# Kernel optimization log

Hardware: AMD Instinct MI355X
Metric: run time of the kernel (lower is better)

## Reference

```python
import jax, jax.numpy as jnp
import numpy as np

B, T, H = 4096, 2048, 64  # batch, max seq len, hidden size
IN = 1                    # decoder input hardcoded to width 1 in source
BOT = 3                   # latent bottleneck (linear_enc: H->3, linear_dec: 3->H)


def setup_inputs() -> dict:
    key = jax.random.key(0)
    ks = jax.random.split(key, 16)
    s = 1.0 / np.sqrt(H)
    u = lambda k, shape: jax.random.uniform(k, shape, jnp.float32, -s, s)
    padded = jax.random.normal(ks[0], (B, T, IN), jnp.float32)
    seq_lengths = jax.random.randint(ks[1], (B,), 1, T + 1).at[0].set(T)  # max == T (static unroll)
    return {
        "padded": padded,
        "seq_lengths": seq_lengths,
        # encoder LSTM (gate order i,f,g,o like torch); biases b_ih+b_hh fused
        "enc_Wih": u(ks[2], (4 * H, IN)),
        "enc_Whh": u(ks[3], (4 * H, H)),
        "enc_b":   u(ks[4], (4 * H,)),
        # encoder bottleneck linear H->3
        "enc_linW": u(ks[5], (BOT, H)),
        "enc_linb": u(ks[6], (BOT,)),
        # decoder expand linear 3->H
        "dec_linW": u(ks[7], (H, BOT)),
        "dec_linb": u(ks[8], (H,)),
        # decoder LSTM
        "dec_Wih": u(ks[9], (4 * H, IN)),
        "dec_Whh": u(ks[10], (4 * H, H)),
        "dec_b":   u(ks[11], (4 * H,)),
        # output linear H->1
        "outW": u(ks[12], (IN, H)),
        "outb": u(ks[13], (IN,)),
    }


def _lstm_cell(x, h, c, Wih, Whh, b):
    g = x @ Wih.T + h @ Whh.T + b
    i, f, gg, o = jnp.split(g, 4, axis=-1)
    c = jax.nn.sigmoid(f) * c + jax.nn.sigmoid(i) * jnp.tanh(gg)
    h = jax.nn.sigmoid(o) * jnp.tanh(c)
    return h, c


def reference(padded, seq_lengths, enc_Wih, enc_Whh, enc_b, enc_linW, enc_linb,
              dec_linW, dec_linb, dec_Wih, dec_Whh, dec_b, outW, outb):
    Bn, Tn, _ = padded.shape
    Hn = enc_Whh.shape[1]
    xs = jnp.transpose(padded, (1, 0, 2))                       # (T, B, 1)
    mask = jnp.arange(Tn)[:, None] < seq_lengths[None, :]        # (T, B)

    # ---- encoder: packed semantics == freeze (h,c) past each seq's length ----
    h0 = jnp.zeros((Bn, Hn), padded.dtype)
    def enc_step(carry, xm):
        h, c = carry
        x, m = xm
        nh, nc = _lstm_cell(x, h, c, enc_Wih, enc_Whh, enc_b)
        m = m[:, None]
        return (jnp.where(m, nh, h), jnp.where(m, nc, c)), None
    (h, c), _ = jax.lax.scan(enc_step, (h0, h0), (xs, mask))

    hz = jax.nn.sigmoid(h @ enc_linW.T + enc_linb)               # (B, 3) latent

    hd = hz @ dec_linW.T + dec_linb                              # (B, H)
    x0 = jnp.zeros((Bn, 1), padded.dtype)
    def dec_step(carry, _):
        x, hh, cc = carry
        nh, nc = _lstm_cell(x, hh, cc, dec_Wih, dec_Whh, dec_b)
        y = nh @ outW.T + outb
        return (y, nh, nc), y
    _, ys = jax.lax.scan(dec_step, (x0, hd, c), None, length=Tn)  # (T, B, 1)
    output = jnp.transpose(ys, (1, 0, 2))                         # (B, T, 1)

    # ---- masked MSE ----
    maskf = mask.T[:, :, None].astype(padded.dtype)               # (B, T, 1)
    loss = (((padded - output) ** 2) * maskf).sum() / maskf.sum()
    return loss, padded, output, hz[None]
```

## Files before the change

### kernel.cpp

```cpp
#include <hip/hip_runtime.h>

#define B 4096
#define T 2048
#define H 64
#define NBATCH 16
#define NB (B / NBATCH)
#define NTHREADS 512

typedef __attribute__((ext_vector_type(8))) short short8;
typedef __attribute__((ext_vector_type(4))) float f32x4;

__device__ __forceinline__ float ex2(float x) { return __builtin_amdgcn_exp2f(x); }
__device__ __forceinline__ unsigned short f2bf(float f) {
    unsigned u = __builtin_bit_cast(unsigned, f);
    u += 0x7fffu + ((u >> 16) & 1u);
    return (unsigned short)(u >> 16);
}
__device__ __forceinline__ unsigned pk_bf16(float a, float b) {
    unsigned r;
    asm("v_cvt_pk_bf16_f32 %0, %1, %2" : "=v"(r) : "v"(a), "v"(b));
    return r;
}
__device__ __forceinline__ void lds_barrier() {
    asm volatile("s_waitcnt lgkmcnt(0)\n\ts_barrier" ::: "memory");
}

__device__ __forceinline__ void cellstep(const f32x4 z, float& cs, float& hs, bool act) {
    const float KE = -1.4426950408889634f;
    const float KT = -2.8853900817779268f;
    float pf = ex2(KE * z[1]);
    float f_ = __builtin_amdgcn_rcpf(1.0f + pf);
    float p0 = ex2(KE * z[0]);
    float v_ = ex2(KT * z[2]);
    float ig = (1.0f - v_) * __builtin_amdgcn_rcpf((1.0f + p0) * (1.0f + v_));
    float cn = __builtin_fmaf(f_, cs, ig);
    float cc = fminf(15.0f, fmaxf(-15.0f, cn));
    float s_ = ex2(KE * z[3]);
    float r_ = ex2(KT * cc);
    float hn = (1.0f - r_) * __builtin_amdgcn_rcpf((1.0f + s_) * (1.0f + r_));
    if (act) { cs = cn; hs = hn; }
}

extern "C" __global__ void __launch_bounds__(NTHREADS, 2)
enc_kernel(const float* __restrict__ padded, const int* __restrict__ seq_len,
           const float* __restrict__ Wih, const float* __restrict__ Whh,
           const float* __restrict__ bias,
           float* __restrict__ h_out, float* __restrict__ c_out)
{
    __shared__ unsigned short hX[2][NBATCH][72];
    __shared__ int slen[NBATCH];

    const int tid = threadIdx.x;
    const int w = tid >> 6, L = tid & 63, lo = L & 15, hi = L >> 4;
    const int b0 = blockIdx.x * NBATCH;
    const int unitA = w * 8 + 2 * hi;
    const int unitB = unitA + 1;

    short8 af[2][2];
    #pragma unroll
    for (int rt = 0; rt < 2; ++rt) {
        const int G = (lo & 3) * 64 + w * 8 + 2 * (lo >> 2) + rt;
        #pragma unroll
        for (int kk = 0; kk < 2; ++kk) {
            const float* src = Whh + (long)G * H + kk * 32 + hi * 8;
            short8 f;
            #pragma unroll
            for (int j = 0; j < 8; ++j) f[j] = (short)f2bf(src[j]);
            af[rt][kk] = f;
        }
    }
    float b_g[2][4], wi_g[2][4];
    #pragma unroll
    for (int rt = 0; rt < 2; ++rt)
        #pragma unroll
        for (int r = 0; r < 4; ++r) {
            const int G2 = r * 64 + w * 8 + 2 * hi + rt;
            b_g[rt][r] = bias[G2];
            wi_g[rt][r] = Wih[G2];
        }

    for (int idx = tid; idx < NBATCH * 64; idx += NTHREADS)
        hX[0][idx >> 6][idx & 63] = 0;
    if (tid < NBATCH) slen[tid] = seq_len[b0 + tid];
    lds_barrier();

    int maxlen = 1;
    #pragma unroll
    for (int i = 0; i < NBATCH; ++i) maxlen = max(maxlen, slen[i]);
    const int len_lo = slen[lo];

    const float* xrow = padded + (long)(b0 + lo) * T;
    f32x4 xc = *(const f32x4*)(xrow);
    f32x4 xn = *(const f32x4*)(xrow + 4);

    float csA = 0.f, hsA = 0.f, csB = 0.f, hsB = 0.f;

#define ESTEP(P, XI)                                                          \
    {                                                                         \
        const float x = xc[XI];                                               \
        short8 hb0 = *(const short8*)&hX[P][lo][hi * 8];                      \
        short8 hb1 = *(const short8*)&hX[P][lo][32 + hi * 8];                 \
        f32x4 z0 = {b_g[0][0] + wi_g[0][0] * x, b_g[0][1] + wi_g[0][1] * x,   \
                    b_g[0][2] + wi_g[0][2] * x, b_g[0][3] + wi_g[0][3] * x};  \
        f32x4 z1 = {b_g[1][0] + wi_g[1][0] * x, b_g[1][1] + wi_g[1][1] * x,   \
                    b_g[1][2] + wi_g[1][2] * x, b_g[1][3] + wi_g[1][3] * x};  \
        z0 = __builtin_amdgcn_mfma_f32_16x16x32_bf16(af[0][0], hb0, z0, 0,0,0); \
        z1 = __builtin_amdgcn_mfma_f32_16x16x32_bf16(af[1][0], hb0, z1, 0,0,0); \
        z0 = __builtin_amdgcn_mfma_f32_16x16x32_bf16(af[0][1], hb1, z0, 0,0,0); \
        z1 = __builtin_amdgcn_mfma_f32_16x16x32_bf16(af[1][1], hb1, z1, 0,0,0); \
        const bool act = (t + XI) < len_lo;                                   \
        cellstep(z0, csA, hsA, act);                                          \
        cellstep(z1, csB, hsB, act);                                          \
        *(unsigned*)&hX[(P) ^ 1][lo][unitA] = pk_bf16(hsA, hsB);              \
        lds_barrier();                                                        \
    }

    for (int t = 0; t < maxlen; t += 4) {
        int nb = t + 8; if (nb > T - 4) nb = T - 4;
        f32x4 xf = *(const f32x4*)(xrow + nb);
        ESTEP(0, 0) ESTEP(1, 1) ESTEP(0, 2) ESTEP(1, 3)
        xc = xn; xn = xf;
    }
#undef ESTEP

    *(float2*)&h_out[(long)(b0 + lo) * H + unitA] = make_float2(hsA, hsB);
    *(float2*)&c_out[(long)(b0 + lo) * H + unitA] = make_float2(csA, csB);
}

extern "C" __global__ void __launch_bounds__(256)
mid_kernel(const float* __restrict__ h_enc,
           const float* __restrict__ eW, const float* __restrict__ eb,
           const float* __restrict__ dW, const float* __restrict__ db,
           const float* __restrict__ outW, const float* __restrict__ outb,
           float* __restrict__ hz_out, float* __restrict__ hd_out,
           float* __restrict__ y0c)
{
    int b = blockIdx.x * blockDim.x + threadIdx.x;
    if (b >= B) return;
    const float* h = h_enc + (long)b * H;
    float hz[3];
    #pragma unroll
    for (int j = 0; j < 3; ++j) {
        float s = eb[j];
        for (int k = 0; k < H; ++k) s += h[k] * eW[j*H + k];
        hz[j] = 1.0f / (1.0f + __builtin_expf(-s));
        hz_out[b*3 + j] = hz[j];
    }
    float y0 = outb[0];
    for (int u = 0; u < H; ++u) {
        float hd = db[u] + hz[0]*dW[u*3] + hz[1]*dW[u*3+1] + hz[2]*dW[u*3+2];
        hd_out[(long)b*H + u] = hd;
        y0 += outW[u] * hd;
    }
    y0c[b] = y0;
}

extern "C" __global__ void __launch_bounds__(NTHREADS, 2)
dec_kernel(const float* __restrict__ hd, const float* __restrict__ c_in,
           const float* __restrict__ Wih, const float* __restrict__ Whh,
           const float* __restrict__ bias, const float* __restrict__ outW,
           const float* __restrict__ outb, const float* __restrict__ y0c,
           float* __restrict__ y_out)
{
    __shared__ unsigned short hX[2][NBATCH][72];

    const int tid = threadIdx.x;
    const int w = tid >> 6, L = tid & 63, lo = L & 15, hi = L >> 4;
    const int b0 = blockIdx.x * NBATCH;
    const int unitA = w * 8 + 2 * hi;
    const int unitB = unitA + 1;

    short8 af[2][2];
    #pragma unroll
    for (int rt = 0; rt < 2; ++rt) {
        const int G = (lo & 3) * 64 + w * 8 + 2 * (lo >> 2) + rt;
        const float wir = Wih[G];
        #pragma unroll
        for (int kk = 0; kk < 2; ++kk) {
            const float* src = Whh + (long)G * H + kk * 32 + hi * 8;
            const float* ow  = outW + kk * 32 + hi * 8;
            short8 f;
            #pragma unroll
            for (int j = 0; j < 8; ++j) f[j] = (short)f2bf(src[j] + wir * ow[j]);
            af[rt][kk] = f;
        }
    }
    const float outb_s = outb[0];
    const float y0 = y0c[b0 + lo];
    float zb[2][4], corr[2][4];
    #pragma unroll
    for (int rt = 0; rt < 2; ++rt)
        #pragma unroll
        for (int r = 0; r < 4; ++r) {
            const int G2 = r * 64 + w * 8 + 2 * hi + rt;
            zb[rt][r] = bias[G2] + Wih[G2] * outb_s;
            corr[rt][r] = Wih[G2] * y0;
        }

    short8 ya[2];
    #pragma unroll
    for (int kk = 0; kk < 2; ++kk) {
        short8 f = (short8)0;
        if (lo == 0)
            #pragma unroll
            for (int j = 0; j < 8; ++j) f[j] = (short)f2bf(outW[kk*32 + hi*8 + j]);
        ya[kk] = f;
    }

    for (int idx = tid; idx < NBATCH * 64; idx += NTHREADS)
        hX[0][idx >> 6][idx & 63] = f2bf(hd[(long)(b0 + (idx >> 6)) * H + (idx & 63)]);
    float2 c2 = *(const float2*)&c_in[(long)(b0 + lo) * H + unitA];
    float csA = c2.x, csB = c2.y, hsA = 0.f, hsB = 0.f;
    lds_barrier();

#define DSTEP(P, CORR, TT)                                                    \
    {                                                                         \
        short8 hb0 = *(const short8*)&hX[P][lo][hi * 8];                      \
        short8 hb1 = *(const short8*)&hX[P][lo][32 + hi * 8];                 \
        f32x4 z0 = {zb[0][0], zb[0][1], zb[0][2], zb[0][3]};                  \
        f32x4 z1 = {zb[1][0], zb[1][1], zb[1][2], zb[1][3]};                  \
        z0 = __builtin_amdgcn_mfma_f32_16x16x32_bf16(af[0][0], hb0, z0, 0,0,0); \
        z1 = __builtin_amdgcn_mfma_f32_16x16x32_bf16(af[1][0], hb0, z1, 0,0,0); \
        z0 = __builtin_amdgcn_mfma_f32_16x16x32_bf16(af[0][1], hb1, z0, 0,0,0); \
        z1 = __builtin_amdgcn_mfma_f32_16x16x32_bf16(af[1][1], hb1, z1, 0,0,0); \
        if (w == ((TT) & 7)) {      \
            f32x4 zy = {outb_s, outb_s, outb_s, outb_s};                      \
            zy = __builtin_amdgcn_mfma_f32_16x16x32_bf16(ya[0], hb0, zy, 0,0,0); \
            zy = __builtin_amdgcn_mfma_f32_16x16x32_bf16(ya[1], hb1, zy, 0,0,0); \
            if ((TT) > 0 && hi == 0)                                          \
                y_out[(long)(b0 + lo) * T + ((TT) - 1)] = zy[0];              \
        }                                                                     \
        if (CORR) {                                                           \
            _Pragma("unroll")                                                 \
            for (int r = 0; r < 4; ++r) { z0[r] -= corr[0][r]; z1[r] -= corr[1][r]; } \
        }                                                                     \
        cellstep(z0, csA, hsA, true);                                         \
        cellstep(z1, csB, hsB, true);                                         \
        *(unsigned*)&hX[(P) ^ 1][lo][unitA] = pk_bf16(hsA, hsB);              \
        lds_barrier();                                                        \
    }

    DSTEP(0, 1, 0) DSTEP(1, 0, 1) DSTEP(0, 0, 2) DSTEP(1, 0, 3)
    for (int t = 4; t < T; t += 4) {
        DSTEP(0, 0, t) DSTEP(1, 0, t + 1) DSTEP(0, 0, t + 2) DSTEP(1, 0, t + 3)
    }
#undef DSTEP

    if (w == 0) {
        short8 hb0 = *(const short8*)&hX[0][lo][hi * 8];
        short8 hb1 = *(const short8*)&hX[0][lo][32 + hi * 8];
        f32x4 zy = {outb_s, outb_s, outb_s, outb_s};
        zy = __builtin_amdgcn_mfma_f32_16x16x32_bf16(ya[0], hb0, zy, 0,0,0);
        zy = __builtin_amdgcn_mfma_f32_16x16x32_bf16(ya[1], hb1, zy, 0,0,0);
        if (hi == 0) y_out[(long)(b0 + lo) * T + (T - 1)] = zy[0];
    }
}

extern "C" __global__ void __launch_bounds__(256)
loss_kernel(const float* __restrict__ padded, const float* __restrict__ y,
            const int* __restrict__ seq_len, float* __restrict__ acc2)
{
    const long n4 = (long)B * T / 4;
    long i0 = (long)(blockIdx.x * blockDim.x + threadIdx.x);
    long stride = (long)gridDim.x * blockDim.x;
    float s = 0.f, cnt = 0.f;
    for (long i = i0; i < n4; i += stride) {
        int b = (int)(i >> 9);
        int t = (int)(i & 511) * 4;
        int len = seq_len[b];
        f32x4 pv = *(const f32x4*)&padded[i * 4];
        f32x4 yv = *(const f32x4*)&y[i * 4];
        #pragma unroll
        for (int e = 0; e < 4; ++e)
            if (t + e < len) { float d = pv[e] - yv[e]; s += d * d; cnt += 1.0f; }
    }
    for (int m = 1; m < 64; m <<= 1) { s += __shfl_xor(s, m); cnt += __shfl_xor(cnt, m); }
    if ((threadIdx.x & 63) == 0) { atomicAdd(&acc2[0], s); atomicAdd(&acc2[1], cnt); }
}

extern "C" __global__ void fin_kernel(const float* __restrict__ acc2, float* __restrict__ out)
{
    out[0] = acc2[0] / acc2[1];
}

extern "C" void kernel_launch(void* const* d_in, const int* in_sizes, int n_in,
                              void* d_out, int out_size, void* d_ws, size_t ws_size,
                              hipStream_t stream)
{
    const float* padded = (const float*)d_in[0];
    const int*   seq    = (const int*)  d_in[1];
    const float* eWih   = (const float*)d_in[2];
    const float* eWhh   = (const float*)d_in[3];
    const float* eb     = (const float*)d_in[4];
    const float* elW    = (const float*)d_in[5];
    const float* elb    = (const float*)d_in[6];
    const float* dlW    = (const float*)d_in[7];
    const float* dlb    = (const float*)d_in[8];
    const float* dWih   = (const float*)d_in[9];
    const float* dWhh   = (const float*)d_in[10];
    const float* db     = (const float*)d_in[11];
    const float* outW   = (const float*)d_in[12];
    const float* outb   = (const float*)d_in[13];
    float* out = (float*)d_out;

    float* ws    = (float*)d_ws;
    float* h_enc = ws;
    float* c_enc = ws + (long)B * H;
    float* hd    = ws + 2L * B * H;
    float* y0c   = ws + 3L * B * H;
    float* acc2  = ws + 3L * B * H + B;

    float* out_pad = out + 1;
    float* out_y   = out + 1 + (long)B * T;
    float* out_hz  = out + 1 + 2L * (long)B * T;

    hipMemcpyAsync(out_pad, padded, (long)B * T * sizeof(float),
                   hipMemcpyDeviceToDevice, stream);
    hipMemsetAsync(acc2, 0, 2 * sizeof(float), stream);

    enc_kernel<<<NB, NTHREADS, 0, stream>>>(padded, seq, eWih, eWhh, eb, h_enc, c_enc);
    mid_kernel<<<B / 256, 256, 0, stream>>>(h_enc, elW, elb, dlW, dlb, outW, outb,
                                            out_hz, hd, y0c);
    dec_kernel<<<NB, NTHREADS, 0, stream>>>(hd, c_enc, dWih, dWhh, db, outW, outb, y0c, out_y);
    loss_kernel<<<1024, 256, 0, stream>>>(padded, out_y, seq, acc2);
    fin_kernel<<<1, 1, 0, stream>>>(acc2, out);
}
```

Before: 1.806 ms.

## Split LSTM blocks into two independent 4-wave groups with LDS counter sync

```diff
diff --git a/kernel.cpp b/kernel.cpp
--- a/kernel.cpp
+++ b/kernel.cpp
@@ -23,6 +23,11 @@
 }
 __device__ __forceinline__ void lds_barrier() {
     asm volatile("s_waitcnt lgkmcnt(0)\n\ts_barrier" ::: "memory");
+}
+__device__ __forceinline__ void gsync(unsigned* c, unsigned tgt, int lane) {
+    if (lane == 0)
+        __hip_atomic_fetch_add(c, 1u, __ATOMIC_RELEASE, __HIP_MEMORY_SCOPE_WORKGROUP);
+    while (__hip_atomic_load(c, __ATOMIC_ACQUIRE, __HIP_MEMORY_SCOPE_WORKGROUP) < tgt) {}
 }
 
 __device__ __forceinline__ void cellstep(const f32x4 z, float& cs, float& hs, bool act) {
@@ -47,72 +52,88 @@
            const float* __restrict__ bias,
            float* __restrict__ h_out, float* __restrict__ c_out)
 {
-    __shared__ unsigned short hX[2][NBATCH][72];
+    __shared__ unsigned short hX[2][2][8][72];
     __shared__ int slen[NBATCH];
+    __shared__ unsigned cnt[2];
 
     const int tid = threadIdx.x;
     const int w = tid >> 6, L = tid & 63, lo = L & 15, hi = L >> 4;
+    const int g = w >> 2, k = w & 3;
     const int b0 = blockIdx.x * NBATCH;
-    const int unitA = w * 8 + 2 * hi;
-    const int unitB = unitA + 1;
-
-    short8 af[2][2];
-    #pragma unroll
-    for (int rt = 0; rt < 2; ++rt) {
-        const int G = (lo & 3) * 64 + w * 8 + 2 * (lo >> 2) + rt;
+    const int cb = lo & 7;
+    const int unitL = 16 * k + 8 * (lo >> 3) + 2 * hi;
+
+    short8 af[4][2];
+    #pragma unroll
+    for (int t4 = 0; t4 < 4; ++t4) {
+        const int G = (lo & 3) * 64 + 16 * k + 8 * (t4 >> 1) + 2 * (lo >> 2) + (t4 & 1);
         #pragma unroll
         for (int kk = 0; kk < 2; ++kk) {
             const float* src = Whh + (long)G * H + kk * 32 + hi * 8;
             short8 f;
             #pragma unroll
             for (int j = 0; j < 8; ++j) f[j] = (short)f2bf(src[j]);
-            af[rt][kk] = f;
+            af[t4][kk] = f;
         }
     }
-    float b_g[2][4], wi_g[2][4];
-    #pragma unroll
-    for (int rt = 0; rt < 2; ++rt)
+    float b_g[4][4], wi_g[4][4];
+    #pragma unroll
+    for (int t4 = 0; t4 < 4; ++t4)
         #pragma unroll
         for (int r = 0; r < 4; ++r) {
-            const int G2 = r * 64 + w * 8 + 2 * hi + rt;
-            b_g[rt][r] = bias[G2];
-            wi_g[rt][r] = Wih[G2];
+            const int G2 = r * 64 + 16 * k + 8 * (t4 >> 1) + 2 * hi + (t4 & 1);
+            b_g[t4][r] = bias[G2];
+            wi_g[t4][r] = Wih[G2];
         }
 
-    for (int idx = tid; idx < NBATCH * 64; idx += NTHREADS)
-        hX[0][idx >> 6][idx & 63] = 0;
+    for (int idx = tid; idx < 2 * 2 * 8 * 72; idx += NTHREADS)
+        ((unsigned short*)hX)[idx] = 0;
     if (tid < NBATCH) slen[tid] = seq_len[b0 + tid];
+    if (tid < 2) cnt[tid] = 0;
     lds_barrier();
+    if (g == 1) __builtin_amdgcn_s_sleep(8);
 
     int maxlen = 1;
     #pragma unroll
-    for (int i = 0; i < NBATCH; ++i) maxlen = max(maxlen, slen[i]);
-    const int len_lo = slen[lo];
-
-    const float* xrow = padded + (long)(b0 + lo) * T;
+    for (int i = 0; i < 8; ++i) maxlen = max(maxlen, slen[g * 8 + i]);
+    const int len_lo = slen[g * 8 + cb];
+
+    const float* xrow = padded + (long)(b0 + g * 8 + cb) * T;
     f32x4 xc = *(const f32x4*)(xrow);
     f32x4 xn = *(const f32x4*)(xrow + 4);
 
     float csA = 0.f, hsA = 0.f, csB = 0.f, hsB = 0.f;
+    unsigned tgt = 0;
 
 #define ESTEP(P, XI)                                                          \
     {                                                                         \
         const float x = xc[XI];                                               \
-        short8 hb0 = *(const short8*)&hX[P][lo][hi * 8];                      \
-        short8 hb1 = *(const short8*)&hX[P][lo][32 + hi * 8];                 \
-        f32x4 z0 = {b_g[0][0] + wi_g[0][0] * x, b_g[0][1] + wi_g[0][1] * x,   \
+        short8 hb0 = *(const short8*)&hX[g][P][cb][hi * 8];                   \
+        short8 hb1 = *(const short8*)&hX[g][P][cb][32 + hi * 8];              \
+        f32x4 q0 = {b_g[0][0] + wi_g[0][0] * x, b_g[0][1] + wi_g[0][1] * x,   \
                     b_g[0][2] + wi_g[0][2] * x, b_g[0][3] + wi_g[0][3] * x};  \
-        f32x4 z1 = {b_g[1][0] + wi_g[1][0] * x, b_g[1][1] + wi_g[1][1] * x,   \
+        f32x4 q1 = {b_g[1][0] + wi_g[1][0] * x, b_g[1][1] + wi_g[1][1] * x,   \
                     b_g[1][2] + wi_g[1][2] * x, b_g[1][3] + wi_g[1][3] * x};  \
-        z0 = __builtin_amdgcn_mfma_f32_16x16x32_bf16(af[0][0], hb0, z0, 0,0,0); \
-        z1 = __builtin_amdgcn_mfma_f32_16x16x32_bf16(af[1][0], hb0, z1, 0,0,0); \
-        z0 = __builtin_amdgcn_mfma_f32_16x16x32_bf16(af[0][1], hb1, z0, 0,0,0); \
-        z1 = __builtin_amdgcn_mfma_f32_16x16x32_bf16(af[1][1], hb1, z1, 0,0,0); \
+        f32x4 q2 = {b_g[2][0] + wi_g[2][0] * x, b_g[2][1] + wi_g[2][1] * x,   \
+                    b_g[2][2] + wi_g[2][2] * x, b_g[2][3] + wi_g[2][3] * x};  \
+        f32x4 q3 = {b_g[3][0] + wi_g[3][0] * x, b_g[3][1] + wi_g[3][1] * x,   \
+                    b_g[3][2] + wi_g[3][2] * x, b_g[3][3] + wi_g[3][3] * x};  \
+        q0 = __builtin_amdgcn_mfma_f32_16x16x32_bf16(af[0][0], hb0, q0, 0,0,0); \
+        q1 = __builtin_amdgcn_mfma_f32_16x16x32_bf16(af[1][0], hb0, q1, 0,0,0); \
+        q2 = __builtin_amdgcn_mfma_f32_16x16x32_bf16(af[2][0], hb0, q2, 0,0,0); \
+        q3 = __builtin_amdgcn_mfma_f32_16x16x32_bf16(af[3][0], hb0, q3, 0,0,0); \
+        q0 = __builtin_amdgcn_mfma_f32_16x16x32_bf16(af[0][1], hb1, q0, 0,0,0); \
+        q1 = __builtin_amdgcn_mfma_f32_16x16x32_bf16(af[1][1], hb1, q1, 0,0,0); \
+        q2 = __builtin_amdgcn_mfma_f32_16x16x32_bf16(af[2][1], hb1, q2, 0,0,0); \
+        q3 = __builtin_amdgcn_mfma_f32_16x16x32_bf16(af[3][1], hb1, q3, 0,0,0); \
+        const bool rep = lo < 8;                                              \
+        f32x4 zA = rep ? q0 : q2;                                             \
+        f32x4 zB = rep ? q1 : q3;                                             \
         const bool act = (t + XI) < len_lo;                                   \
-        cellstep(z0, csA, hsA, act);                                          \
-        cellstep(z1, csB, hsB, act);                                          \
-        *(unsigned*)&hX[(P) ^ 1][lo][unitA] = pk_bf16(hsA, hsB);              \
-        lds_barrier();                                                        \
+        cellstep(zA, csA, hsA, act);                                          \
+        cellstep(zB, csB, hsB, act);                                          \
+        *(unsigned*)&hX[g][(P) ^ 1][cb][unitL] = pk_bf16(hsA, hsB);           \
+        tgt += 4; gsync(&cnt[g], tgt, L);                                     \
     }
 
     for (int t = 0; t < maxlen; t += 4) {
@@ -123,8 +144,8 @@
     }
 #undef ESTEP
 
-    *(float2*)&h_out[(long)(b0 + lo) * H + unitA] = make_float2(hsA, hsB);
-    *(float2*)&c_out[(long)(b0 + lo) * H + unitA] = make_float2(csA, csB);
+    *(float2*)&h_out[(long)(b0 + g * 8 + cb) * H + unitL] = make_float2(hsA, hsB);
+    *(float2*)&c_out[(long)(b0 + g * 8 + cb) * H + unitL] = make_float2(csA, csB);
 }
 
 extern "C" __global__ void __launch_bounds__(256)
@@ -142,7 +163,7 @@
     #pragma unroll
     for (int j = 0; j < 3; ++j) {
         float s = eb[j];
-        for (int k = 0; k < H; ++k) s += h[k] * eW[j*H + k];
+        for (int kq = 0; kq < H; ++kq) s += h[kq] * eW[j*H + kq];
         hz[j] = 1.0f / (1.0f + __builtin_expf(-s));
         hz_out[b*3 + j] = hz[j];
     }
@@ -162,18 +183,20 @@
            const float* __restrict__ outb, const float* __restrict__ y0c,
            float* __restrict__ y_out)
 {
-    __shared__ unsigned short hX[2][NBATCH][72];
+    __shared__ unsigned short hX[2][2][8][72];
+    __shared__ unsigned cnt[2];
 
     const int tid = threadIdx.x;
     const int w = tid >> 6, L = tid & 63, lo = L & 15, hi = L >> 4;
+    const int g = w >> 2, k = w & 3;
     const int b0 = blockIdx.x * NBATCH;
-    const int unitA = w * 8 + 2 * hi;
-    const int unitB = unitA + 1;
-
-    short8 af[2][2];
-    #pragma unroll
-    for (int rt = 0; rt < 2; ++rt) {
-        const int G = (lo & 3) * 64 + w * 8 + 2 * (lo >> 2) + rt;
+    const int cb = lo & 7;
+    const int unitL = 16 * k + 8 * (lo >> 3) + 2 * hi;
+
+    short8 af[4][2];
+    #pragma unroll
+    for (int t4 = 0; t4 < 4; ++t4) {
+        const int G = (lo & 3) * 64 + 16 * k + 8 * (t4 >> 1) + 2 * (lo >> 2) + (t4 & 1);
         const float wir = Wih[G];
         #pragma unroll
         for (int kk = 0; kk < 2; ++kk) {
@@ -182,20 +205,25 @@
             short8 f;
             #pragma unroll
             for (int j = 0; j < 8; ++j) f[j] = (short)f2bf(src[j] + wir * ow[j]);
-            af[rt][kk] = f;
+            af[t4][kk] = f;
         }
     }
     const float outb_s = outb[0];
-    const float y0 = y0c[b0 + lo];
-    float zb[2][4], corr[2][4];
-    #pragma unroll
-    for (int rt = 0; rt < 2; ++rt)
+    const float y0 = y0c[b0 + g * 8 + cb];
+    float zb[4][4];
+    #pragma unroll
+    for (int t4 = 0; t4 < 4; ++t4)
         #pragma unroll
         for (int r = 0; r < 4; ++r) {
-            const int G2 = r * 64 + w * 8 + 2 * hi + rt;
-            zb[rt][r] = bias[G2] + Wih[G2] * outb_s;
-            corr[rt][r] = Wih[G2] * y0;
+            const int G2 = r * 64 + 16 * k + 8 * (t4 >> 1) + 2 * hi + (t4 & 1);
+            zb[t4][r] = bias[G2] + Wih[G2] * outb_s;
         }
+    float corrA[4], corrB[4];
+    #pragma unroll
+    for (int r = 0; r < 4; ++r) {
+        corrA[r] = Wih[r * 64 + unitL] * y0;
+        corrB[r] = Wih[r * 64 + unitL + 1] * y0;
+    }
 
     short8 ya[2];
     #pragma unroll
@@ -207,37 +235,51 @@
         ya[kk] = f;
     }
 
-    for (int idx = tid; idx < NBATCH * 64; idx += NTHREADS)
-        hX[0][idx >> 6][idx & 63] = f2bf(hd[(long)(b0 + (idx >> 6)) * H + (idx & 63)]);
-    float2 c2 = *(const float2*)&c_in[(long)(b0 + lo) * H + unitA];
+    for (int idx = tid; idx < NBATCH * 64; idx += NTHREADS) {
+        int m = idx >> 6, col = idx & 63;
+        hX[m >> 3][0][m & 7][col] = f2bf(hd[(long)(b0 + m) * H + col]);
+    }
+    if (tid < 2) cnt[tid] = 0;
+    float2 c2 = *(const float2*)&c_in[(long)(b0 + g * 8 + cb) * H + unitL];
     float csA = c2.x, csB = c2.y, hsA = 0.f, hsB = 0.f;
     lds_barrier();
+    if (g == 1) __builtin_amdgcn_s_sleep(8);
+    unsigned tgt = 0;
 
 #define DSTEP(P, CORR, TT)                                                    \
     {                                                                         \
-        short8 hb0 = *(const short8*)&hX[P][lo][hi * 8];                      \
-        short8 hb1 = *(const short8*)&hX[P][lo][32 + hi * 8];                 \
-        f32x4 z0 = {zb[0][0], zb[0][1], zb[0][2], zb[0][3]};                  \
-        f32x4 z1 = {zb[1][0], zb[1][1], zb[1][2], zb[1][3]};                  \
-        z0 = __builtin_amdgcn_mfma_f32_16x16x32_bf16(af[0][0], hb0, z0, 0,0,0); \
-        z1 = __builtin_amdgcn_mfma_f32_16x16x32_bf16(af[1][0], hb0, z1, 0,0,0); \
-        z0 = __builtin_amdgcn_mfma_f32_16x16x32_bf16(af[0][1], hb1, z0, 0,0,0); \
-        z1 = __builtin_amdgcn_mfma_f32_16x16x32_bf16(af[1][1], hb1, z1, 0,0,0); \
-        if (w == ((TT) & 7)) {      \
+        short8 hb0 = *(const short8*)&hX[g][P][cb][hi * 8];                   \
+        short8 hb1 = *(const short8*)&hX[g][P][cb][32 + hi * 8];              \
+        f32x4 q0 = {zb[0][0], zb[0][1], zb[0][2], zb[0][3]};                  \
+        f32x4 q1 = {zb[1][0], zb[1][1], zb[1][2], zb[1][3]};                  \
+        f32x4 q2 = {zb[2][0], zb[2][1], zb[2][2], zb[2][3]};                  \
+        f32x4 q3 = {zb[3][0], zb[3][1], zb[3][2], zb[3][3]};                  \
+        q0 = __builtin_amdgcn_mfma_f32_16x16x32_bf16(af[0][0], hb0, q0, 0,0,0); \
+        q1 = __builtin_amdgcn_mfma_f32_16x16x32_bf16(af[1][0], hb0, q1, 0,0,0); \
+        q2 = __builtin_amdgcn_mfma_f32_16x16x32_bf16(af[2][0], hb0, q2, 0,0,0); \
+        q3 = __builtin_amdgcn_mfma_f32_16x16x32_bf16(af[3][0], hb0, q3, 0,0,0); \
+        q0 = __builtin_amdgcn_mfma_f32_16x16x32_bf16(af[0][1], hb1, q0, 0,0,0); \
+        q1 = __builtin_amdgcn_mfma_f32_16x16x32_bf16(af[1][1], hb1, q1, 0,0,0); \
+        q2 = __builtin_amdgcn_mfma_f32_16x16x32_bf16(af[2][1], hb1, q2, 0,0,0); \
+        q3 = __builtin_amdgcn_mfma_f32_16x16x32_bf16(af[3][1], hb1, q3, 0,0,0); \
+        if (k == ((TT) & 3)) {      \
             f32x4 zy = {outb_s, outb_s, outb_s, outb_s};                      \
             zy = __builtin_amdgcn_mfma_f32_16x16x32_bf16(ya[0], hb0, zy, 0,0,0); \
             zy = __builtin_amdgcn_mfma_f32_16x16x32_bf16(ya[1], hb1, zy, 0,0,0); \
-            if ((TT) > 0 && hi == 0)                                          \
-                y_out[(long)(b0 + lo) * T + ((TT) - 1)] = zy[0];              \
+            if ((TT) > 0 && hi == 0 && lo < 8)                                \
+                y_out[(long)(b0 + g * 8 + lo) * T + ((TT) - 1)] = zy[0];      \
         }                                                                     \
+        const bool rep = lo < 8;                                              \
+        f32x4 zA = rep ? q0 : q2;                                             \
+        f32x4 zB = rep ? q1 : q3;                                             \
         if (CORR) {                                                           \
             _Pragma("unroll")                                                 \
-            for (int r = 0; r < 4; ++r) { z0[r] -= corr[0][r]; z1[r] -= corr[1][r]; } \
+            for (int r = 0; r < 4; ++r) { zA[r] -= corrA[r]; zB[r] -= corrB[r]; } \
         }                                                                     \
-        cellstep(z0, csA, hsA, true);                                         \
-        cellstep(z1, csB, hsB, true);                                         \
-        *(unsigned*)&hX[(P) ^ 1][lo][unitA] = pk_bf16(hsA, hsB);              \
-        lds_barrier();                                                        \
+        cellstep(zA, csA, hsA, true);                                         \
+        cellstep(zB, csB, hsB, true);                                         \
+        *(unsigned*)&hX[g][(P) ^ 1][cb][unitL] = pk_bf16(hsA, hsB);           \
+        tgt += 4; gsync(&cnt[g], tgt, L);                                     \
     }
 
     DSTEP(0, 1, 0) DSTEP(1, 0, 1) DSTEP(0, 0, 2) DSTEP(1, 0, 3)
@@ -246,13 +288,13 @@
     }
 #undef DSTEP
 
-    if (w == 0) {
-        short8 hb0 = *(const short8*)&hX[0][lo][hi * 8];
-        short8 hb1 = *(const short8*)&hX[0][lo][32 + hi * 8];
+    if (k == 0) {
+        short8 hb0 = *(const short8*)&hX[g][0][cb][hi * 8];
+        short8 hb1 = *(const short8*)&hX[g][0][cb][32 + hi * 8];
         f32x4 zy = {outb_s, outb_s, outb_s, outb_s};
         zy = __builtin_amdgcn_mfma_f32_16x16x32_bf16(ya[0], hb0, zy, 0,0,0);
         zy = __builtin_amdgcn_mfma_f32_16x16x32_bf16(ya[1], hb1, zy, 0,0,0);
-        if (hi == 0) y_out[(long)(b0 + lo) * T + (T - 1)] = zy[0];
+        if (hi == 0 && lo < 8) y_out[(long)(b0 + g * 8 + lo) * T + (T - 1)] = zy[0];
     }
 }
 
@@ -263,7 +305,7 @@
     const long n4 = (long)B * T / 4;
     long i0 = (long)(blockIdx.x * blockDim.x + threadIdx.x);
     long stride = (long)gridDim.x * blockDim.x;
-    float s = 0.f, cnt = 0.f;
+    float s = 0.f, cntv = 0.f;
     for (long i = i0; i < n4; i += stride) {
         int b = (int)(i >> 9);
         int t = (int)(i & 511) * 4;
@@ -272,10 +314,10 @@
         f32x4 yv = *(const f32x4*)&y[i * 4];
         #pragma unroll
         for (int e = 0; e < 4; ++e)
-            if (t + e < len) { float d = pv[e] - yv[e]; s += d * d; cnt += 1.0f; }
-    }
-    for (int m = 1; m < 64; m <<= 1) { s += __shfl_xor(s, m); cnt += __shfl_xor(cnt, m); }
-    if ((threadIdx.x & 63) == 0) { atomicAdd(&acc2[0], s); atomicAdd(&acc2[1], cnt); }
+            if (t + e < len) { float d = pv[e] - yv[e]; s += d * d; cntv += 1.0f; }
+    }
+    for (int m = 1; m < 64; m <<= 1) { s += __shfl_xor(s, m); cntv += __shfl_xor(cntv, m); }
+    if ((threadIdx.x & 63) == 0) { atomicAdd(&acc2[0], s); atomicAdd(&acc2[1], cntv); }
 }
 
 extern "C" __global__ void fin_kernel(const float* __restrict__ acc2, float* __restrict__ out)
```

Result: slower. 2.155 ms (+19.3%).

## Halve waves per block so each wave computes four gate tiles

Applied to the files above, without the earlier changes.

```diff
diff --git a/kernel.cpp b/kernel.cpp
--- a/kernel.cpp
+++ b/kernel.cpp
@@ -5,7 +5,7 @@
 #define H 64
 #define NBATCH 16
 #define NB (B / NBATCH)
-#define NTHREADS 512
+#define NTHREADS 256
 
 typedef __attribute__((ext_vector_type(8))) short short8;
 typedef __attribute__((ext_vector_type(4))) float f32x4;
@@ -41,7 +41,7 @@
     if (act) { cs = cn; hs = hn; }
 }
 
-extern "C" __global__ void __launch_bounds__(NTHREADS, 2)
+extern "C" __global__ void __launch_bounds__(NTHREADS, 1)
 enc_kernel(const float* __restrict__ padded, const int* __restrict__ seq_len,
            const float* __restrict__ Wih, const float* __restrict__ Whh,
            const float* __restrict__ bias,
@@ -53,30 +53,30 @@
     const int tid = threadIdx.x;
     const int w = tid >> 6, L = tid & 63, lo = L & 15, hi = L >> 4;
     const int b0 = blockIdx.x * NBATCH;
-    const int unitA = w * 8 + 2 * hi;
-    const int unitB = unitA + 1;
-
-    short8 af[2][2];
-    #pragma unroll
-    for (int rt = 0; rt < 2; ++rt) {
-        const int G = (lo & 3) * 64 + w * 8 + 2 * (lo >> 2) + rt;
+    const int uA = 16 * w + 2 * hi;
+    const int uC = uA + 8;
+
+    short8 af[4][2];
+    #pragma unroll
+    for (int q = 0; q < 4; ++q) {
+        const int G = (lo & 3) * 64 + 16 * w + 8 * (q >> 1) + 2 * (lo >> 2) + (q & 1);
         #pragma unroll
         for (int kk = 0; kk < 2; ++kk) {
             const float* src = Whh + (long)G * H + kk * 32 + hi * 8;
             short8 f;
             #pragma unroll
             for (int j = 0; j < 8; ++j) f[j] = (short)f2bf(src[j]);
-            af[rt][kk] = f;
+            af[q][kk] = f;
         }
     }
-    float b_g[2][4], wi_g[2][4];
-    #pragma unroll
-    for (int rt = 0; rt < 2; ++rt)
+    float b_g[4][4], wi_g[4][4];
+    #pragma unroll
+    for (int q = 0; q < 4; ++q)
         #pragma unroll
         for (int r = 0; r < 4; ++r) {
-            const int G2 = r * 64 + w * 8 + 2 * hi + rt;
-            b_g[rt][r] = bias[G2];
-            wi_g[rt][r] = Wih[G2];
+            const int G2 = r * 64 + 16 * w + 8 * (q >> 1) + 2 * hi + (q & 1);
+            b_g[q][r] = bias[G2];
+            wi_g[q][r] = Wih[G2];
         }
 
     for (int idx = tid; idx < NBATCH * 64; idx += NTHREADS)
@@ -93,7 +93,8 @@
     f32x4 xc = *(const f32x4*)(xrow);
     f32x4 xn = *(const f32x4*)(xrow + 4);
 
-    float csA = 0.f, hsA = 0.f, csB = 0.f, hsB = 0.f;
+    float cs0 = 0.f, hs0 = 0.f, cs1 = 0.f, hs1 = 0.f;
+    float cs2 = 0.f, hs2 = 0.f, cs3 = 0.f, hs3 = 0.f;
 
 #define ESTEP(P, XI)                                                          \
     {                                                                         \
@@ -104,14 +105,25 @@
                     b_g[0][2] + wi_g[0][2] * x, b_g[0][3] + wi_g[0][3] * x};  \
         f32x4 z1 = {b_g[1][0] + wi_g[1][0] * x, b_g[1][1] + wi_g[1][1] * x,   \
                     b_g[1][2] + wi_g[1][2] * x, b_g[1][3] + wi_g[1][3] * x};  \
+        f32x4 z2 = {b_g[2][0] + wi_g[2][0] * x, b_g[2][1] + wi_g[2][1] * x,   \
+                    b_g[2][2] + wi_g[2][2] * x, b_g[2][3] + wi_g[2][3] * x};  \
+        f32x4 z3 = {b_g[3][0] + wi_g[3][0] * x, b_g[3][1] + wi_g[3][1] * x,   \
+                    b_g[3][2] + wi_g[3][2] * x, b_g[3][3] + wi_g[3][3] * x};  \
         z0 = __builtin_amdgcn_mfma_f32_16x16x32_bf16(af[0][0], hb0, z0, 0,0,0); \
         z1 = __builtin_amdgcn_mfma_f32_16x16x32_bf16(af[1][0], hb0, z1, 0,0,0); \
+        z2 = __builtin_amdgcn_mfma_f32_16x16x32_bf16(af[2][0], hb0, z2, 0,0,0); \
+        z3 = __builtin_amdgcn_mfma_f32_16x16x32_bf16(af[3][0], hb0, z3, 0,0,0); \
         z0 = __builtin_amdgcn_mfma_f32_16x16x32_bf16(af[0][1], hb1, z0, 0,0,0); \
         z1 = __builtin_amdgcn_mfma_f32_16x16x32_bf16(af[1][1], hb1, z1, 0,0,0); \
+        z2 = __builtin_amdgcn_mfma_f32_16x16x32_bf16(af[2][1], hb1, z2, 0,0,0); \
+        z3 = __builtin_amdgcn_mfma_f32_16x16x32_bf16(af[3][1], hb1, z3, 0,0,0); \
         const bool act = (t + XI) < len_lo;                                   \
-        cellstep(z0, csA, hsA, act);                                          \
-        cellstep(z1, csB, hsB, act);                                          \
-        *(unsigned*)&hX[(P) ^ 1][lo][unitA] = pk_bf16(hsA, hsB);              \
+        cellstep(z0, cs0, hs0, act);                                          \
+        cellstep(z1, cs1, hs1, act);                                          \
+        cellstep(z2, cs2, hs2, act);                                          \
+        cellstep(z3, cs3, hs3, act);                                          \
+        *(unsigned*)&hX[(P) ^ 1][lo][uA] = pk_bf16(hs0, hs1);                 \
+        *(unsigned*)&hX[(P) ^ 1][lo][uC] = pk_bf16(hs2, hs3);                 \
         lds_barrier();                                                        \
     }
 
@@ -123,8 +135,10 @@
     }
 #undef ESTEP
 
-    *(float2*)&h_out[(long)(b0 + lo) * H + unitA] = make_float2(hsA, hsB);
-    *(float2*)&c_out[(long)(b0 + lo) * H + unitA] = make_float2(csA, csB);
+    *(float2*)&h_out[(long)(b0 + lo) * H + uA] = make_float2(hs0, hs1);
+    *(float2*)&h_out[(long)(b0 + lo) * H + uC] = make_float2(hs2, hs3);
+    *(float2*)&c_out[(long)(b0 + lo) * H + uA] = make_float2(cs0, cs1);
+    *(float2*)&c_out[(long)(b0 + lo) * H + uC] = make_float2(cs2, cs3);
 }
 
 extern "C" __global__ void __launch_bounds__(256)
@@ -155,7 +169,7 @@
     y0c[b] = y0;
 }
 
-extern "C" __global__ void __launch_bounds__(NTHREADS, 2)
+extern "C" __global__ void __launch_bounds__(NTHREADS, 1)
 dec_kernel(const float* __restrict__ hd, const float* __restrict__ c_in,
            const float* __restrict__ Wih, const float* __restrict__ Whh,
            const float* __restrict__ bias, const float* __restrict__ outW,
@@ -167,13 +181,13 @@
     const int tid = threadIdx.x;
     const int w = tid >> 6, L = tid & 63, lo = L & 15, hi = L >> 4;
     const int b0 = blockIdx.x * NBATCH;
-    const int unitA = w * 8 + 2 * hi;
-    const int unitB = unitA + 1;
-
-    short8 af[2][2];
-    #pragma unroll
-    for (int rt = 0; rt < 2; ++rt) {
-        const int G = (lo & 3) * 64 + w * 8 + 2 * (lo >> 2) + rt;
+    const int uA = 16 * w + 2 * hi;
+    const int uC = uA + 8;
+
+    short8 af[4][2];
+    #pragma unroll
+    for (int q = 0; q < 4; ++q) {
+        const int G = (lo & 3) * 64 + 16 * w + 8 * (q >> 1) + 2 * (lo >> 2) + (q & 1);
         const float wir = Wih[G];
         #pragma unroll
         for (int kk = 0; kk < 2; ++kk) {
@@ -182,19 +196,19 @@
             short8 f;
             #pragma unroll
             for (int j = 0; j < 8; ++j) f[j] = (short)f2bf(src[j] + wir * ow[j]);
-            af[rt][kk] = f;
+            af[q][kk] = f;
         }
     }
     const float outb_s = outb[0];
     const float y0 = y0c[b0 + lo];
-    float zb[2][4], corr[2][4];
-    #pragma unroll
-    for (int rt = 0; rt < 2; ++rt)
+    float zb[4][4], corr[4][4];
+    #pragma unroll
+    for (int q = 0; q < 4; ++q)
         #pragma unroll
         for (int r = 0; r < 4; ++r) {
-            const int G2 = r * 64 + w * 8 + 2 * hi + rt;
-            zb[rt][r] = bias[G2] + Wih[G2] * outb_s;
-            corr[rt][r] = Wih[G2] * y0;
+            const int G2 = r * 64 + 16 * w + 8 * (q >> 1) + 2 * hi + (q & 1);
+            zb[q][r] = bias[G2] + Wih[G2] * outb_s;
+            corr[q][r] = Wih[G2] * y0;
         }
 
     short8 ya[2];
@@ -209,8 +223,10 @@
 
     for (int idx = tid; idx < NBATCH * 64; idx += NTHREADS)
         hX[0][idx >> 6][idx & 63] = f2bf(hd[(long)(b0 + (idx >> 6)) * H + (idx & 63)]);
-    float2 c2 = *(const float2*)&c_in[(long)(b0 + lo) * H + unitA];
-    float csA = c2.x, csB = c2.y, hsA = 0.f, hsB = 0.f;
+    float2 cA = *(const float2*)&c_in[(long)(b0 + lo) * H + uA];
+    float2 cC = *(const float2*)&c_in[(long)(b0 + lo) * H + uC];
+    float cs0 = cA.x, cs1 = cA.y, cs2 = cC.x, cs3 = cC.y;
+    float hs0 = 0.f, hs1 = 0.f, hs2 = 0.f, hs3 = 0.f;
     lds_barrier();
 
 #define DSTEP(P, CORR, TT)                                                    \
@@ -219,11 +235,17 @@
         short8 hb1 = *(const short8*)&hX[P][lo][32 + hi * 8];                 \
         f32x4 z0 = {zb[0][0], zb[0][1], zb[0][2], zb[0][3]};                  \
         f32x4 z1 = {zb[1][0], zb[1][1], zb[1][2], zb[1][3]};                  \
+        f32x4 z2 = {zb[2][0], zb[2][1], zb[2][2], zb[2][3]};                  \
+        f32x4 z3 = {zb[3][0], zb[3][1], zb[3][2], zb[3][3]};                  \
         z0 = __builtin_amdgcn_mfma_f32_16x16x32_bf16(af[0][0], hb0, z0, 0,0,0); \
         z1 = __builtin_amdgcn_mfma_f32_16x16x32_bf16(af[1][0], hb0, z1, 0,0,0); \
+        z2 = __builtin_amdgcn_mfma_f32_16x16x32_bf16(af[2][0], hb0, z2, 0,0,0); \
+        z3 = __builtin_amdgcn_mfma_f32_16x16x32_bf16(af[3][0], hb0, z3, 0,0,0); \
         z0 = __builtin_amdgcn_mfma_f32_16x16x32_bf16(af[0][1], hb1, z0, 0,0,0); \
         z1 = __builtin_amdgcn_mfma_f32_16x16x32_bf16(af[1][1], hb1, z1, 0,0,0); \
-        if (w == ((TT) & 7)) {      \
+        z2 = __builtin_amdgcn_mfma_f32_16x16x32_bf16(af[2][1], hb1, z2, 0,0,0); \
+        z3 = __builtin_amdgcn_mfma_f32_16x16x32_bf16(af[3][1], hb1, z3, 0,0,0); \
+        if (w == ((TT) & 3)) {      \
             f32x4 zy = {outb_s, outb_s, outb_s, outb_s};                      \
             zy = __builtin_amdgcn_mfma_f32_16x16x32_bf16(ya[0], hb0, zy, 0,0,0); \
             zy = __builtin_amdgcn_mfma_f32_16x16x32_bf16(ya[1], hb1, zy, 0,0,0); \
@@ -232,11 +254,17 @@
         }                                                                     \
         if (CORR) {                                                           \
             _Pragma("unroll")                                                 \
-            for (int r = 0; r < 4; ++r) { z0[r] -= corr[0][r]; z1[r] -= corr[1][r]; } \
+            for (int r = 0; r < 4; ++r) {                                     \
+                z0[r] -= corr[0][r]; z1[r] -= corr[1][r];                     \
+                z2[r] -= corr[2][r]; z3[r] -= corr[3][r];                     \
+            }                                                                 \
         }                                                                     \
-        cellstep(z0, csA, hsA, true);                                         \
-        cellstep(z1, csB, hsB, true);                                         \
-        *(unsigned*)&hX[(P) ^ 1][lo][unitA] = pk_bf16(hsA, hsB);              \
+        cellstep(z0, cs0, hs0, true);                                         \
+        cellstep(z1, cs1, hs1, true);                                         \
+        cellstep(z2, cs2, hs2, true);                                         \
+        cellstep(z3, cs3, hs3, true);                                         \
+        *(unsigned*)&hX[(P) ^ 1][lo][uA] = pk_bf16(hs0, hs1);                 \
+        *(unsigned*)&hX[(P) ^ 1][lo][uC] = pk_bf16(hs2, hs3);                 \
         lds_barrier();                                                        \
     }
 
```

Result: slower. 2.306 ms (+27.7%).

## Remap gate rows so LSTM cell math uses packed two-wide FP32 ops

Applied to the files above, without the earlier changes.

```diff
diff --git a/kernel.cpp b/kernel.cpp
--- a/kernel.cpp
+++ b/kernel.cpp
@@ -9,6 +9,7 @@
 
 typedef __attribute__((ext_vector_type(8))) short short8;
 typedef __attribute__((ext_vector_type(4))) float f32x4;
+typedef __attribute__((ext_vector_type(2))) float f32x2;
 
 __device__ __forceinline__ float ex2(float x) { return __builtin_amdgcn_exp2f(x); }
 __device__ __forceinline__ unsigned short f2bf(float f) {
@@ -21,24 +22,60 @@
     asm("v_cvt_pk_bf16_f32 %0, %1, %2" : "=v"(r) : "v"(a), "v"(b));
     return r;
 }
+__device__ __forceinline__ f32x2 pk_mul(f32x2 a, f32x2 b) {
+    f32x2 d; asm("v_pk_mul_f32 %0, %1, %2" : "=v"(d) : "v"(a), "v"(b)); return d;
+}
+__device__ __forceinline__ f32x2 pk_add(f32x2 a, f32x2 b) {
+    f32x2 d; asm("v_pk_add_f32 %0, %1, %2" : "=v"(d) : "v"(a), "v"(b)); return d;
+}
+__device__ __forceinline__ f32x2 pk_fma(f32x2 a, f32x2 b, f32x2 c) {
+    f32x2 d; asm("v_pk_fma_f32 %0, %1, %2, %3" : "=v"(d) : "v"(a), "v"(b), "v"(c)); return d;
+}
+__device__ __forceinline__ f32x2 pex2(f32x2 a) {
+    float x, y;
+    asm("v_exp_f32 %0, %1" : "=v"(x) : "v"(a.x));
+    asm("v_exp_f32 %0, %1" : "=v"(y) : "v"(a.y));
+    return (f32x2){x, y};
+}
+__device__ __forceinline__ f32x2 prcp(f32x2 a) {
+    float x, y;
+    asm("v_rcp_f32 %0, %1" : "=v"(x) : "v"(a.x));
+    asm("v_rcp_f32 %0, %1" : "=v"(y) : "v"(a.y));
+    return (f32x2){x, y};
+}
 __device__ __forceinline__ void lds_barrier() {
     asm volatile("s_waitcnt lgkmcnt(0)\n\ts_barrier" ::: "memory");
 }
 
-__device__ __forceinline__ void cellstep(const f32x4 z, float& cs, float& hs, bool act) {
-    const float KE = -1.4426950408889634f;
-    const float KT = -2.8853900817779268f;
-    float pf = ex2(KE * z[1]);
-    float f_ = __builtin_amdgcn_rcpf(1.0f + pf);
-    float p0 = ex2(KE * z[0]);
-    float v_ = ex2(KT * z[2]);
-    float ig = (1.0f - v_) * __builtin_amdgcn_rcpf((1.0f + p0) * (1.0f + v_));
-    float cn = __builtin_fmaf(f_, cs, ig);
-    float cc = fminf(15.0f, fmaxf(-15.0f, cn));
-    float s_ = ex2(KE * z[3]);
-    float r_ = ex2(KT * cc);
-    float hn = (1.0f - r_) * __builtin_amdgcn_rcpf((1.0f + s_) * (1.0f + r_));
-    if (act) { cs = cn; hs = hn; }
+__device__ __forceinline__ void cellstep2(const f32x4 z0, const f32x4 z1,
+                                          f32x2& csp, f32x2& hsp, bool act) {
+    const f32x2 ke2  = {-1.4426950408889634f, -1.4426950408889634f};
+    const f32x2 kt2  = {-2.8853900817779268f, -2.8853900817779268f};
+    const f32x2 one2 = {1.0f, 1.0f};
+    const f32x2 mone2= {-1.0f, -1.0f};
+    f32x2 pi = {z0[0], z0[1]}, pf = {z0[2], z0[3]};
+    f32x2 pg = {z1[0], z1[1]}, po = {z1[2], z1[3]};
+    f32x2 ei = pex2(pk_mul(pi, ke2));
+    f32x2 ef = pex2(pk_mul(pf, ke2));
+    f32x2 eg = pex2(pk_mul(pg, kt2));
+    f32x2 eo = pex2(pk_mul(po, ke2));
+    f32x2 t1 = pk_add(ei, one2);
+    f32x2 t3 = pk_add(ef, one2);
+    f32x2 t2 = pk_add(eg, one2);
+    f32x2 u  = pk_fma(eg, mone2, one2);
+    f32x2 m1 = pk_mul(t1, t2);
+    f32x2 D  = pk_mul(m1, t3);
+    f32x2 rD = prcp(D);
+    f32x2 N  = pk_fma(csp, m1, pk_mul(u, t3));
+    f32x2 cn = pk_mul(N, rD);
+    float ccx = fminf(15.f, fmaxf(-15.f, cn.x));
+    float ccy = fminf(15.f, fmaxf(-15.f, cn.y));
+    f32x2 er = pex2(pk_mul((f32x2){ccx, ccy}, kt2));
+    f32x2 t5 = pk_add(er, one2);
+    f32x2 w1 = pk_fma(er, mone2, one2);
+    f32x2 t4 = pk_add(eo, one2);
+    f32x2 hn = pk_mul(w1, prcp(pk_mul(t4, t5)));
+    if (act) { csp = cn; hsp = hn; }
 }
 
 extern "C" __global__ void __launch_bounds__(NTHREADS, 2)
@@ -54,12 +91,11 @@
     const int w = tid >> 6, L = tid & 63, lo = L & 15, hi = L >> 4;
     const int b0 = blockIdx.x * NBATCH;
     const int unitA = w * 8 + 2 * hi;
-    const int unitB = unitA + 1;
 
     short8 af[2][2];
     #pragma unroll
     for (int rt = 0; rt < 2; ++rt) {
-        const int G = (lo & 3) * 64 + w * 8 + 2 * (lo >> 2) + rt;
+        const int G = (rt * 2 + ((lo >> 1) & 1)) * 64 + w * 8 + 2 * (lo >> 2) + (lo & 1);
         #pragma unroll
         for (int kk = 0; kk < 2; ++kk) {
             const float* src = Whh + (long)G * H + kk * 32 + hi * 8;
@@ -74,7 +110,7 @@
     for (int rt = 0; rt < 2; ++rt)
         #pragma unroll
         for (int r = 0; r < 4; ++r) {
-            const int G2 = r * 64 + w * 8 + 2 * hi + rt;
+            const int G2 = (rt * 2 + (r >> 1)) * 64 + unitA + (r & 1);
             b_g[rt][r] = bias[G2];
             wi_g[rt][r] = Wih[G2];
         }
@@ -93,7 +129,7 @@
     f32x4 xc = *(const f32x4*)(xrow);
     f32x4 xn = *(const f32x4*)(xrow + 4);
 
-    float csA = 0.f, hsA = 0.f, csB = 0.f, hsB = 0.f;
+    f32x2 csp = {0.f, 0.f}, hsp = {0.f, 0.f};
 
 #define ESTEP(P, XI)                                                          \
     {                                                                         \
@@ -109,9 +145,8 @@
         z0 = __builtin_amdgcn_mfma_f32_16x16x32_bf16(af[0][1], hb1, z0, 0,0,0); \
         z1 = __builtin_amdgcn_mfma_f32_16x16x32_bf16(af[1][1], hb1, z1, 0,0,0); \
         const bool act = (t + XI) < len_lo;                                   \
-        cellstep(z0, csA, hsA, act);                                          \
-        cellstep(z1, csB, hsB, act);                                          \
-        *(unsigned*)&hX[(P) ^ 1][lo][unitA] = pk_bf16(hsA, hsB);              \
+        cellstep2(z0, z1, csp, hsp, act);                                     \
+        *(unsigned*)&hX[(P) ^ 1][lo][unitA] = pk_bf16(hsp.x, hsp.y);          \
         lds_barrier();                                                        \
     }
 
@@ -123,8 +158,8 @@
     }
 #undef ESTEP
 
-    *(float2*)&h_out[(long)(b0 + lo) * H + unitA] = make_float2(hsA, hsB);
-    *(float2*)&c_out[(long)(b0 + lo) * H + unitA] = make_float2(csA, csB);
+    *(f32x2*)&h_out[(long)(b0 + lo) * H + unitA] = hsp;
+    *(f32x2*)&c_out[(long)(b0 + lo) * H + unitA] = csp;
 }
 
 extern "C" __global__ void __launch_bounds__(256)
@@ -168,12 +203,11 @@
     const int w = tid >> 6, L = tid & 63, lo = L & 15, hi = L >> 4;
     const int b0 = blockIdx.x * NBATCH;
     const int unitA = w * 8 + 2 * hi;
-    const int unitB = unitA + 1;
 
     short8 af[2][2];
     #pragma unroll
     for (int rt = 0; rt < 2; ++rt) {
-        const int G = (lo & 3) * 64 + w * 8 + 2 * (lo >> 2) + rt;
+        const int G = (rt * 2 + ((lo >> 1) & 1)) * 64 + w * 8 + 2 * (lo >> 2) + (lo & 1);
         const float wir = Wih[G];
         #pragma unroll
         for (int kk = 0; kk < 2; ++kk) {
@@ -192,7 +226,7 @@
     for (int rt = 0; rt < 2; ++rt)
         #pragma unroll
         for (int r = 0; r < 4; ++r) {
-            const int G2 = r * 64 + w * 8 + 2 * hi + rt;
+            const int G2 = (rt * 2 + (r >> 1)) * 64 + unitA + (r & 1);
             zb[rt][r] = bias[G2] + Wih[G2] * outb_s;
             corr[rt][r] = Wih[G2] * y0;
         }
@@ -209,8 +243,8 @@
 
     for (int idx = tid; idx < NBATCH * 64; idx += NTHREADS)
         hX[0][idx >> 6][idx & 63] = f2bf(hd[(long)(b0 + (idx >> 6)) * H + (idx & 63)]);
-    float2 c2 = *(const float2*)&c_in[(long)(b0 + lo) * H + unitA];
-    float csA = c2.x, csB = c2.y, hsA = 0.f, hsB = 0.f;
+    f32x2 csp = *(const f32x2*)&c_in[(long)(b0 + lo) * H + unitA];
+    f32x2 hsp = {0.f, 0.f};
     lds_barrier();
 
 #define DSTEP(P, CORR, TT)                                                    \
@@ -234,9 +268,8 @@
             _Pragma("unroll")                                                 \
             for (int r = 0; r < 4; ++r) { z0[r] -= corr[0][r]; z1[r] -= corr[1][r]; } \
         }                                                                     \
-        cellstep(z0, csA, hsA, true);                                         \
-        cellstep(z1, csB, hsB, true);                                         \
-        *(unsigned*)&hX[(P) ^ 1][lo][unitA] = pk_bf16(hsA, hsB);              \
+        cellstep2(z0, z1, csp, hsp, true);                                    \
+        *(unsigned*)&hX[(P) ^ 1][lo][unitA] = pk_bf16(hsp.x, hsp.y);          \
         lds_barrier();                                                        \
     }
 
```

New measurement: 1.748 ms. 1.03x faster.
